# Kernel optimization log

Hardware: AMD Instinct MI355X
Metric: run time of the kernel (lower is better)

## Reference

```python
import jax, jax.numpy as jnp
import numpy as np

B, T, N, D, K, MP = 32, 50, 50000, 128, 16, 50
HID = (D + K) // 2  # WP_1 out features


def _normalize(x, axis=-1, eps=1e-12):
    return x / jnp.maximum(jnp.linalg.norm(x, axis=axis, keepdims=True), eps)


def _layer_norm(x, g, b, eps=1e-6):
    m = jnp.mean(x, axis=-1, keepdims=True)
    v = jnp.var(x, axis=-1, keepdims=True)
    return (x - m) * jax.lax.rsqrt(v + eps) * g + b


def setup_inputs() -> dict:
    key = jax.random.key(0)
    ks = jax.random.split(key, 20)
    std = 0.01
    session = jax.random.randint(ks[0], (B, T), 1, N + 1)  # ids >= 1, no padding
    lengths = jnp.full((B,), T, dtype=jnp.int32)
    isValidSession = jnp.ones((B * T,), dtype=bool)
    inp = {
        'session': session,
        'lengths': lengths,
        'tau': 1,
        'isValidSession': isValidSession,
        'train': 1,
        'I_emb': jax.random.normal(ks[1], (N + 1, D)) * std,
        'P_emb': jax.random.normal(ks[2], (K, D)) * std,
        'E_P_emb': jax.random.normal(ks[3], (MP, D)) * std,
        'E_S_emb': jax.random.normal(ks[4], (MP + 1, D)) * std,
        'V': _normalize(jax.random.normal(ks[5], (K, D))),
        'WP1': jax.random.normal(ks[6], (HID, D)),   # torch Linear weight [out, in]
        'WP2': jax.random.normal(ks[7], (K, HID)),
        'Wq': jax.random.normal(ks[8], (D, D)) / np.sqrt(D),
        'Wk': jax.random.normal(ks[9], (D, D)) / np.sqrt(D),
        'Wv': jax.random.normal(ks[10], (D, D)) / np.sqrt(D),
        'Wo': jax.random.normal(ks[11], (D, D)) / np.sqrt(D),
        'FF1': jax.random.normal(ks[12], (D, D)) / np.sqrt(D),
        'FF2': jax.random.normal(ks[13], (D, D)) / np.sqrt(D),
        'ln1_g': jnp.ones((D,)), 'ln1_b': jnp.zeros((D,)),
        'ln2_g': jnp.ones((D,)), 'ln2_b': jnp.zeros((D,)),
    }
    return inp


def _forward(session, lengths, tau, I_emb, P_emb, E_P_emb, E_S_emb, V,
             WP1, WP2, Wq, Wk, Wv, Wo, FF1, FF2, ln1_g, ln1_b, ln2_g, ln2_b):
    Vn = _normalize(V)                               # forward renormalizes V rows
    lf = lengths.astype(jnp.float32)
    isValidPos = (session != 0).astype(jnp.float32)  # [B,T]
    sess_emb = I_emb[session]                        # [B,T,D]
    EP = E_P_emb[jnp.arange(T) + (MP - T)]           # [T,D]
    es_idx = jnp.maximum(jnp.arange(T)[None, :] + 1 - (T - lengths[:, None]), 0)
    ES = E_S_emb[es_idx]                             # [B,T,D]

    # ---- ProxySelection (dropout in eval mode = identity) ----
    X = isValidPos[..., None] * (sess_emb + EP[None])
    X = jax.nn.leaky_relu(X @ WP1.T, 0.1) @ WP2.T    # [B,T,K]
    fP = jnp.sum(X, axis=1) / lf[:, None]
    pi = jax.nn.softmax(fP / tau, axis=-1)           # [B,K]
    p_s = pi @ P_emb                                 # [B,D]
    v = _normalize(pi @ Vn)                          # [B,D]

    # ---- SIE: single-layer self-attention encoder ----
    Xs = sess_emb + ES
    subseq = jnp.triu(jnp.ones((T, T), dtype=bool), 1)[None]        # causal
    pad = (session == 0)[:, None, :]                                # key padding
    mask = (subseq | pad)
    mask = mask.at[:, :, 0].set(False)
    non_pad = (session != 0).astype(jnp.float32)[..., None]
    q, kk, vv = Xs @ Wq.T, Xs @ Wk.T, Xs @ Wv.T
    scores = jnp.einsum('btd,bsd->bts', q, kk) / np.sqrt(D)
    scores = jnp.where(mask, -1e9, scores)
    attn = jax.nn.softmax(scores, axis=-1)
    h = (attn @ vv) @ Wo.T
    h = _layer_norm(h + Xs, ln1_g, ln1_b) * non_pad
    f = jax.nn.relu(h @ FF1.T) @ FF2.T
    s_s = _layer_norm(f + h, ln2_g, ln2_b) * non_pad                # [B,T,D]

    # project out v component per sample
    s_s_proj = s_s - v[:, None, :] * jnp.sum(v[:, None, :] * s_s, axis=-1, keepdims=True)
    orthogonal = jnp.abs(jnp.sum(v * p_s, axis=-1)) / jnp.linalg.norm(p_s, axis=-1)

    # ---- train_phase: dist(p_s+s_s_proj[b,t], I_proj_b) for all items ----
    # I_proj_b = I - v_b (v_b . I); with ||v_b||=1:
    #   ||F - I_proj||^2 = ||F||^2 - 2(F.I - (F.v)(v.I)) + ||I||^2 - (v.I)^2
    F = p_s[:, None, :] + s_s_proj                   # [B,T,D]
    vI = jnp.einsum('nd,bd->bn', I_emb, v)           # [B,N+1]
    Fv = jnp.einsum('btd,bd->bt', F, v)              # [B,T]
    FI = jnp.einsum('btd,nd->btn', F, I_emb)         # [B,T,N+1]
    Fn2 = jnp.sum(F * F, axis=-1)                    # [B,T]
    In2 = jnp.sum(I_emb * I_emb, axis=-1)[None, :] - vI * vI  # [B,N+1]
    dist = Fn2[..., None] - 2.0 * (FI - Fv[..., None] * vI[:, None, :]) + In2[:, None, :]
    return dist.reshape(B * T, N + 1), orthogonal


def reference(session, lengths, tau, isValidSession, train,
              I_emb, P_emb, E_P_emb, E_S_emb, V,
              WP1, WP2, Wq, Wk, Wv, Wo, FF1, FF2, ln1_g, ln1_b, ln2_g, ln2_b):
    # isValidSession is all-True and train=1: distance rows = all (b,t) pairs
    return _forward(session, lengths, tau, I_emb, P_emb, E_P_emb, E_S_emb, V,
                    WP1, WP2, Wq, Wk, Wv, Wo, FF1, FF2, ln1_g, ln1_b, ln2_g, ln2_b)
```

## Files before the change

### kernel.cpp

```cpp
#include <hip/hip_runtime.h>
#include <math.h>

#define B   32
#define T   50
#define N1  50001
#define D   128
#define KP  16
#define MP  50
#define HID 72
#define BT  (B*T)

typedef __attribute__((ext_vector_type(8))) short short8v;
typedef __attribute__((ext_vector_type(4))) float f32x4;

__device__ __forceinline__ unsigned short f2bf(float x) {
    unsigned u = __float_as_uint(x);
    u += 0x7fffu + ((u >> 16) & 1u);
    return (unsigned short)(u >> 16);
}

__device__ __forceinline__ float blockReduceSum128(float val, volatile float* sbuf) {
    for (int off = 32; off > 0; off >>= 1) val += __shfl_down(val, off, 64);
    __syncthreads();
    if ((threadIdx.x & 63) == 0) sbuf[threadIdx.x >> 6] = val;
    __syncthreads();
    return sbuf[0] + sbuf[1];
}

__global__ void k_fused_emb(const int* __restrict__ session,
                            const int* __restrict__ lengths,
                            const float* __restrict__ I_emb,
                            const float* __restrict__ EP_emb,
                            const float* __restrict__ ES_emb,
                            const float* __restrict__ WP1,
                            const float* __restrict__ WP2,
                            const float* __restrict__ Wq,
                            const float* __restrict__ Wk,
                            const float* __restrict__ Wv,
                            float* __restrict__ X2,
                            float* __restrict__ xs_o, float* __restrict__ q_o,
                            float* __restrict__ k_o, float* __restrict__ v_o) {
    int bt = blockIdx.x; int b = bt / T; int t = bt % T;
    int tid = threadIdx.x;
    __shared__ __align__(16) float x[D];
    __shared__ __align__(16) float xs[D];
    __shared__ float h[HID];
    int sid = session[bt];
    float ie = I_emb[(size_t)sid * D + tid];
    float xv_ = (sid != 0) ? (ie + EP_emb[(t + MP - T) * D + tid]) : 0.f;
    int es = t + 1 - (T - lengths[b]); if (es < 0) es = 0;
    float xsv = ie + ES_emb[es * D + tid];
    x[tid] = xv_;
    xs[tid] = xsv;
    __syncthreads();
    float aq = 0.f, ak = 0.f, av = 0.f;
    {
        const float4* wq4 = (const float4*)(Wq + tid * D);
        const float4* wk4 = (const float4*)(Wk + tid * D);
        const float4* wv4 = (const float4*)(Wv + tid * D);
        const float4* x4  = (const float4*)xs;
        #pragma unroll 8
        for (int k = 0; k < D / 4; ++k) {
            float4 xv = x4[k];
            float4 a = wq4[k], bq = wk4[k], c = wv4[k];
            aq += xv.x * a.x + xv.y * a.y + xv.z * a.z + xv.w * a.w;
            ak += xv.x * bq.x + xv.y * bq.y + xv.z * bq.z + xv.w * bq.w;
            av += xv.x * c.x + xv.y * c.y + xv.z * c.z + xv.w * c.w;
        }
    }
    if (tid < HID) {
        float acc = 0.f;
        const float4* w4 = (const float4*)(WP1 + tid * D);
        const float4* x4 = (const float4*)x;
        #pragma unroll 8
        for (int k = 0; k < D / 4; ++k) {
            float4 w = w4[k]; float4 xv = x4[k];
            acc += xv.x * w.x + xv.y * w.y + xv.z * w.z + xv.w * w.w;
        }
        h[tid] = acc > 0.f ? acc : 0.1f * acc;
    }
    xs_o[bt * D + tid] = xsv;
    q_o[bt * D + tid] = aq; k_o[bt * D + tid] = ak; v_o[bt * D + tid] = av;
    __syncthreads();
    if (tid < KP) {
        float acc = 0.f;
        const float* w = WP2 + tid * HID;
        for (int k = 0; k < HID; ++k) acc += h[k] * w[k];
        X2[bt * KP + tid] = acc;
    }
}

__global__ void k_proxy_head(const float* __restrict__ X2,
                             const int* __restrict__ lengths,
                             const int* __restrict__ tau_i,
                             const float* __restrict__ P_emb,
                             const float* __restrict__ V,
                             float* __restrict__ ps_o,
                             float* __restrict__ v_o,
                             float* __restrict__ orth_o) {
    int b = blockIdx.x; int tid = threadIdx.x;
    __shared__ float pi[KP];
    __shared__ float vn[KP];
    __shared__ float sbuf[2];
    float tau = (float)tau_i[0];
    float lf = (float)lengths[b];
    if (tid < KP) {
        float s = 0.f;
        for (int t = 0; t < T; ++t) s += X2[(b * T + t) * KP + tid];
        pi[tid] = (s / lf) / tau;
    }
    if (tid < KP) {
        float s = 0.f;
        for (int d = 0; d < D; ++d) { float z = V[tid * D + d]; s += z * z; }
        vn[tid] = fmaxf(sqrtf(s), 1e-12f);
    }
    __syncthreads();
    if (tid == 0) {
        float m = pi[0];
        for (int k = 1; k < KP; ++k) m = fmaxf(m, pi[k]);
        float s = 0.f;
        for (int k = 0; k < KP; ++k) { float e = expf(pi[k] - m); pi[k] = e; s += e; }
        for (int k = 0; k < KP; ++k) pi[k] /= s;
    }
    __syncthreads();
    float p = 0.f, vt = 0.f;
    for (int k = 0; k < KP; ++k) {
        p  += pi[k] * P_emb[k * D + tid];
        vt += pi[k] * (V[k * D + tid] / vn[k]);
    }
    float vsq = blockReduceSum128(vt * vt, sbuf);
    float vv = vt / fmaxf(sqrtf(vsq), 1e-12f);
    float psq = blockReduceSum128(p * p, sbuf);
    float dvp = blockReduceSum128(vv * p, sbuf);
    ps_o[b * D + tid] = p;
    v_o[b * D + tid] = vv;
    if (tid == 0) orth_o[b] = fabsf(dvp) / sqrtf(psq);
}

__global__ void k_fused_attn(const int* __restrict__ session,
                             const float* __restrict__ q,
                             const float* __restrict__ kk,
                             const float* __restrict__ vv,
                             const float* __restrict__ xs,
                             const float* __restrict__ Wo,
                             const float* __restrict__ g1, const float* __restrict__ b1,
                             const float* __restrict__ FF1, const float* __restrict__ FF2,
                             const float* __restrict__ g2, const float* __restrict__ b2,
                             const float* __restrict__ ps, const float* __restrict__ v,
                             short* __restrict__ G16, float* __restrict__ Fn2) {
    int bt = blockIdx.x; int b = bt / T; int t = bt % T;
    int tid = threadIdx.x;
    __shared__ __align__(16) float qs[D];
    __shared__ __align__(16) float buf1[D];
    __shared__ __align__(16) float buf2[D];
    __shared__ float attn[64];
    __shared__ float sbuf[2];
    qs[tid] = q[bt * D + tid];
    __syncthreads();
    if (tid < T) {
        int s = tid;
        bool allowed = (s == 0) || ((s <= t) && (session[b * T + s] != 0));
        float sc = -1e9f;
        if (allowed) {
            float a = 0.f;
            const float4* kr = (const float4*)(kk + (size_t)(b * T + s) * D);
            const float4* q4 = (const float4*)qs;
            #pragma unroll 8
            for (int d = 0; d < D / 4; ++d) {
                float4 kv = kr[d]; float4 qv = q4[d];
                a += qv.x * kv.x + qv.y * kv.y + qv.z * kv.z + qv.w * kv.w;
            }
            sc = a * 0.088388347648318447f;
        }
        attn[s] = sc;
    }
    __syncthreads();
    if (tid < 64) {
        float vsc = (tid < T) ? attn[tid] : -1e30f;
        float m = vsc;
        for (int off = 32; off > 0; off >>= 1) m = fmaxf(m, __shfl_xor(m, off, 64));
        float e = (tid < T) ? expf(vsc - m) : 0.f;
        float ssum = e;
        for (int off = 32; off > 0; off >>= 1) ssum += __shfl_xor(ssum, off, 64);
        if (tid < T) attn[tid] = e / ssum;
    }
    __syncthreads();
    float acc = 0.f;
    for (int s = 0; s < T; ++s) acc += attn[s] * vv[(size_t)(b * T + s) * D + tid];
    buf1[tid] = acc;
    __syncthreads();
    float a = 0.f;
    {
        const float4* w4 = (const float4*)(Wo + tid * D);
        const float4* h4 = (const float4*)buf1;
        #pragma unroll 8
        for (int k = 0; k < D / 4; ++k) {
            float4 w = w4[k]; float4 hv = h4[k];
            a += hv.x * w.x + hv.y * w.y + hv.z * w.z + hv.w * w.w;
        }
    }
    float x1 = a + xs[bt * D + tid];
    float mean = blockReduceSum128(x1, sbuf) * (1.f / D);
    float dx = x1 - mean;
    float var = blockReduceSum128(dx * dx, sbuf) * (1.f / D);
    float hx = (dx * rsqrtf(var + 1e-6f) * g1[tid] + b1[tid]) * ((session[bt] != 0) ? 1.f : 0.f);
    buf2[tid] = hx;
    __syncthreads();
    float a1 = 0.f;
    {
        const float4* w4 = (const float4*)(FF1 + tid * D);
        const float4* h4 = (const float4*)buf2;
        #pragma unroll 8
        for (int k = 0; k < D / 4; ++k) {
            float4 w = w4[k]; float4 hv = h4[k];
            a1 += hv.x * w.x + hv.y * w.y + hv.z * w.z + hv.w * w.w;
        }
    }
    __syncthreads();
    buf1[tid] = fmaxf(a1, 0.f);
    __syncthreads();
    float f = 0.f;
    {
        const float4* w4 = (const float4*)(FF2 + tid * D);
        const float4* t4 = (const float4*)buf1;
        #pragma unroll 8
        for (int k = 0; k < D / 4; ++k) {
            float4 w = w4[k]; float4 tv = t4[k];
            f += tv.x * w.x + tv.y * w.y + tv.z * w.z + tv.w * w.w;
        }
    }
    float x2 = f + hx;
    float mean2 = blockReduceSum128(x2, sbuf) * (1.f / D);
    float dx2 = x2 - mean2;
    float var2 = blockReduceSum128(dx2 * dx2, sbuf) * (1.f / D);
    float ss = dx2 * rsqrtf(var2 + 1e-6f) * g2[tid] + b2[tid];
    ss *= (session[bt] != 0) ? 1.f : 0.f;
    float vb = v[b * D + tid];
    float vs = blockReduceSum128(vb * ss, sbuf);
    float ssp = ss - vb * vs;
    float Fd = ps[b * D + tid] + ssp;
    float Fv = blockReduceSum128(Fd * vb, sbuf);
    float Gd = Fd - Fv * vb;
    float fn2 = blockReduceSum128(Fd * Fd, sbuf);
    G16[bt * D + tid] = (short)f2bf(Gd);
    if (tid == 0) Fn2[bt] = fn2;
}

#define LDK 136

__global__ __launch_bounds__(256) void k_item_mfma(const float* __restrict__ I,
                                                   const float* __restrict__ v,
                                                   float* __restrict__ In2pb,
                                                   unsigned short* __restrict__ I16) {
    __shared__ __align__(16) short Is[64][LDK];
    __shared__ __align__(16) short Vs[32][LDK];
    __shared__ float sq[64][4];
    __shared__ float in2[64];
    int n0 = blockIdx.x * 64;
    int tid = threadIdx.x;
    {
        int vr = tid >> 3;
        int vc = (tid & 7) * 16;
        const float4* src = (const float4*)&v[vr * D + vc];
        #pragma unroll
        for (int s = 0; s < 4; ++s) {
            float4 f = src[s];
            ushort4 u;
            u.x = f2bf(f.x); u.y = f2bf(f.y); u.z = f2bf(f.z); u.w = f2bf(f.w);
            *(ushort4*)&Vs[vr][vc + s * 4] = u;
        }
    }
    {
        int r = tid >> 2;
        int qq = tid & 3;
        int n = n0 + r;
        float ss = 0.f;
        if (n < N1) {
            const float4* src = (const float4*)&I[(size_t)n * D + qq * 32];
            #pragma unroll
            for (int s = 0; s < 8; ++s) {
                float4 f = src[s];
                ss += f.x * f.x + f.y * f.y + f.z * f.z + f.w * f.w;
                ushort4 u;
                u.x = f2bf(f.x); u.y = f2bf(f.y); u.z = f2bf(f.z); u.w = f2bf(f.w);
                *(ushort4*)&Is[r][qq * 32 + s * 4] = u;
                *(ushort4*)&I16[(size_t)n * D + qq * 32 + s * 4] = u;
            }
        } else {
            #pragma unroll
            for (int s = 0; s < 8; ++s)
                *(ushort4*)&Is[r][qq * 32 + s * 4] = make_ushort4(0, 0, 0, 0);
        }
        sq[r][qq] = ss;
    }
    __syncthreads();
    if (tid < 64) in2[tid] = sq[tid][0] + sq[tid][1] + sq[tid][2] + sq[tid][3];
    __syncthreads();
    int w = tid >> 6, l = tid & 63, lr = l & 15, lg = l >> 4;
    f32x4 acc[2] = {{0.f,0.f,0.f,0.f},{0.f,0.f,0.f,0.f}};
    short8v af[4];
    #pragma unroll
    for (int ks = 0; ks < 4; ++ks)
        af[ks] = *(const short8v*)&Is[w * 16 + lr][ks * 32 + lg * 8];
    #pragma unroll
    for (int nt = 0; nt < 2; ++nt) {
        #pragma unroll
        for (int ks = 0; ks < 4; ++ks) {
            short8v bf = *(const short8v*)&Vs[nt * 16 + lr][ks * 32 + lg * 8];
            acc[nt] = __builtin_amdgcn_mfma_f32_16x16x32_bf16(af[ks], bf, acc[nt], 0, 0, 0);
        }
    }
    #pragma unroll
    for (int nt = 0; nt < 2; ++nt) {
        int b = nt * 16 + lr;
        #pragma unroll
        for (int i = 0; i < 4; ++i) {
            int item = w * 16 + lg * 4 + i;
            int n = n0 + item;
            if (n < N1) {
                float dvi = acc[nt][i];
                In2pb[(size_t)b * N1 + n] = in2[item] - dvi * dvi;
            }
        }
    }
}

#define BN 128
__global__ __launch_bounds__(256) void k_dist_mfma(const short* __restrict__ G16,
                                                   const unsigned short* __restrict__ I16,
                                                   const float* __restrict__ Fn2,
                                                   const float* __restrict__ In2pb,
                                                   float* __restrict__ out) {
    __shared__ __align__(16) short Bs[BN][LDK];
    __shared__ float in2s[B][BN];
    int n0  = blockIdx.x * BN;
    int rt0 = (blockIdx.y == 0) ? 0 : 7;
    int rt1 = (blockIdx.y == 0) ? 7 : 13;
    int tid = threadIdx.x;
    {
        int r  = tid >> 1;
        int c0 = (tid & 1) * 64;
        int n = n0 + r;
        #pragma unroll
        for (int s = 0; s < 8; ++s) {
            short8v bv = {};
            if (n < N1) bv = *(const short8v*)&I16[(size_t)n * D + c0 + s * 8];
            *(short8v*)&Bs[r][c0 + s * 8] = bv;
        }
    }
    for (int i = tid; i < B * BN; i += 256) {
        int bb = i >> 7;
        int cl = i & (BN - 1);
        int col = n0 + cl;
        in2s[bb][cl] = (col < N1) ? In2pb[(size_t)bb * N1 + col] : 0.f;
    }
    __syncthreads();
    int w  = tid >> 6;
    int l  = tid & 63;
    int lr = l & 15;
    int lg = l >> 4;
    for (int rt = rt0; rt < rt1; ++rt) {
        int bt0 = rt * 128;
        #pragma unroll
        for (int mi = 0; mi < 2; ++mi) {
            int rbase = bt0 + w * 32 + mi * 16;
            short8v af[4];
            const short* arow = &G16[(size_t)(rbase + lr) * D];
            #pragma unroll
            for (int ks = 0; ks < 4; ++ks)
                af[ks] = *(const short8v*)&arow[ks * 32 + lg * 8];
            f32x4 acc[8];
            #pragma unroll
            for (int nt = 0; nt < 8; ++nt) acc[nt] = (f32x4){0.f, 0.f, 0.f, 0.f};
            #pragma unroll
            for (int nt = 0; nt < 8; ++nt) {
                #pragma unroll
                for (int ks = 0; ks < 4; ++ks) {
                    short8v bf = *(const short8v*)&Bs[nt * 16 + lr][ks * 32 + lg * 8];
                    acc[nt] = __builtin_amdgcn_mfma_f32_16x16x32_bf16(af[ks], bf, acc[nt], 0, 0, 0);
                }
            }
            int rb = rbase + lg * 4;
            if (rb < BT) {
                float4 fn4 = *(const float4*)&Fn2[rb];
                float fnv[4] = {fn4.x, fn4.y, fn4.z, fn4.w};
                #pragma unroll
                for (int i = 0; i < 4; ++i) {
                    int row = rb + i;
                    int bb = row / T;
                    float* orow = out + (size_t)row * N1 + n0;
                    #pragma unroll
                    for (int nt = 0; nt < 8; ++nt) {
                        int cl = nt * 16 + lr;
                        if (n0 + cl < N1) orow[cl] = fnv[i] + in2s[bb][cl] - 2.f * acc[nt][i];
                    }
                }
            }
        }
    }
}

extern "C" void kernel_launch(void* const* d_in, const int* in_sizes, int n_in,
                              void* d_out, int out_size, void* d_ws, size_t ws_size,
                              hipStream_t stream) {
    const int*   session = (const int*)d_in[0];
    const int*   lengths = (const int*)d_in[1];
    const int*   tau     = (const int*)d_in[2];
    const float* I_emb   = (const float*)d_in[5];
    const float* P_emb   = (const float*)d_in[6];
    const float* EP      = (const float*)d_in[7];
    const float* ES      = (const float*)d_in[8];
    const float* V       = (const float*)d_in[9];
    const float* WP1     = (const float*)d_in[10];
    const float* WP2     = (const float*)d_in[11];
    const float* Wq      = (const float*)d_in[12];
    const float* Wk      = (const float*)d_in[13];
    const float* Wv      = (const float*)d_in[14];
    const float* Wo      = (const float*)d_in[15];
    const float* FF1     = (const float*)d_in[16];
    const float* FF2     = (const float*)d_in[17];
    const float* g1      = (const float*)d_in[18];
    const float* b1      = (const float*)d_in[19];
    const float* g2      = (const float*)d_in[20];
    const float* b2      = (const float*)d_in[21];
    float* out = (float*)d_out;
    float* ws  = (float*)d_ws;

    float* wsX2   = ws;
    float* wsPs   = wsX2 + 25600;
    float* wsV    = wsPs + 4096;
    float* wsXs   = wsV + 4096;
    float* wsQ    = wsXs + 204800;
    float* wsK    = wsQ + 204800;
    float* wsVv   = wsK + 204800;
    float* wsFn2  = wsVv + 204800;
    float* wsIn2  = wsFn2 + 1600;
    short* wsG16  = (short*)(wsIn2 + 1600032);
    unsigned short* wsI16 = (unsigned short*)(wsG16 + 212992);

    float* orth_out = out + (size_t)BT * N1;

    k_fused_emb <<<BT, 128, 0, stream>>>(session, lengths, I_emb, EP, ES,
                                         WP1, WP2, Wq, Wk, Wv,
                                         wsX2, wsXs, wsQ, wsK, wsVv);
    k_proxy_head<<<B, 128, 0, stream>>>(wsX2, lengths, tau, P_emb, V, wsPs, wsV, orth_out);
    k_fused_attn<<<BT, 128, 0, stream>>>(session, wsQ, wsK, wsVv, wsXs,
                                         Wo, g1, b1, FF1, FF2, g2, b2,
                                         wsPs, wsV, wsG16, wsFn2);
    k_item_mfma <<<(N1 + 63) / 64, 256, 0, stream>>>(I_emb, wsV, wsIn2, wsI16);
    dim3 gdist((N1 + BN - 1) / BN, 2);
    k_dist_mfma <<<gdist, 256, 0, stream>>>(wsG16, wsI16, wsFn2, wsIn2, out);
}
```

Baseline: 265.2 us.

## Fuse embedding, proxy head and transformer layer into one per-batch kernel

Replaces three kernels (per-position embedding/QKV, per-batch proxy head, per-position attention+FFN) with one kernel launched once per batch element, 256 threads each. All intermediates (xs, q, k, v, hidden, attention output) stay in LDS. Each weight row is reused across 10 sequence positions per tile. This removes two launches and the global round-trips for Q/K/V/X2/ps. The cost is that parallelism drops to 32 blocks, several stages use only 16–128 of the 256 threads, and the kernel needs a large LDS footprint, so this part may run serially on a few CUs.

```diff
diff --git a/kernel.cpp b/kernel.cpp
--- a/kernel.cpp
+++ b/kernel.cpp
@@ -19,231 +19,303 @@
     return (unsigned short)(u >> 16);
 }
 
-__device__ __forceinline__ float blockReduceSum128(float val, volatile float* sbuf) {
-    for (int off = 32; off > 0; off >>= 1) val += __shfl_down(val, off, 64);
-    __syncthreads();
-    if ((threadIdx.x & 63) == 0) sbuf[threadIdx.x >> 6] = val;
-    __syncthreads();
-    return sbuf[0] + sbuf[1];
+__device__ __forceinline__ float halfReduce256(float v, int half, int lane, volatile float* rbuf) {
+    for (int off = 32; off > 0; off >>= 1) v += __shfl_down(v, off, 64);
+    __syncthreads();
+    if ((lane & 63) == 0) rbuf[half * 2 + (lane >> 6)] = v;
+    __syncthreads();
+    return rbuf[half * 2] + rbuf[half * 2 + 1];
 }
 
-__global__ void k_fused_emb(const int* __restrict__ session,
-                            const int* __restrict__ lengths,
-                            const float* __restrict__ I_emb,
-                            const float* __restrict__ EP_emb,
-                            const float* __restrict__ ES_emb,
-                            const float* __restrict__ WP1,
-                            const float* __restrict__ WP2,
-                            const float* __restrict__ Wq,
-                            const float* __restrict__ Wk,
-                            const float* __restrict__ Wv,
-                            float* __restrict__ X2,
-                            float* __restrict__ xs_o, float* __restrict__ q_o,
-                            float* __restrict__ k_o, float* __restrict__ v_o) {
-    int bt = blockIdx.x; int b = bt / T; int t = bt % T;
+__global__ __launch_bounds__(256) void k_mega(const int* __restrict__ session,
+                                              const int* __restrict__ lengths,
+                                              const int* __restrict__ tau_i,
+                                              const float* __restrict__ I_emb,
+                                              const float* __restrict__ EP,
+                                              const float* __restrict__ ES,
+                                              const float* __restrict__ WP1,
+                                              const float* __restrict__ WP2,
+                                              const float* __restrict__ P_emb,
+                                              const float* __restrict__ V,
+                                              const float* __restrict__ Wq,
+                                              const float* __restrict__ Wk,
+                                              const float* __restrict__ Wv,
+                                              const float* __restrict__ Wo,
+                                              const float* __restrict__ g1, const float* __restrict__ b1,
+                                              const float* __restrict__ FF1, const float* __restrict__ FF2,
+                                              const float* __restrict__ g2, const float* __restrict__ b2,
+                                              short* __restrict__ G16,
+                                              float* __restrict__ Fn2,
+                                              float* __restrict__ v_o,
+                                              float* __restrict__ orth_o) {
+    __shared__ __align__(16) float xsS[T][132];
+    __shared__ __align__(16) float qS[T][132];
+    __shared__ __align__(16) float kS[T][132];
+    __shared__ __align__(16) float vS[T][132];
+    __shared__ __align__(16) float aoS[T][132];
+    __shared__ __align__(16) float hS[T][76];
+    __shared__ float X2S[T][KP];
+    __shared__ float attnS[2][64];
+    __shared__ float psS[D];
+    __shared__ float vvS[D];
+    __shared__ float piS[KP];
+    __shared__ float vnS[KP];
+    __shared__ int   sessS[T];
+    __shared__ float rbuf[4];
+
+    int b = blockIdx.x;
     int tid = threadIdx.x;
-    __shared__ __align__(16) float x[D];
-    __shared__ __align__(16) float xs[D];
-    __shared__ float h[HID];
-    int sid = session[bt];
-    float ie = I_emb[(size_t)sid * D + tid];
-    float xv_ = (sid != 0) ? (ie + EP_emb[(t + MP - T) * D + tid]) : 0.f;
-    int es = t + 1 - (T - lengths[b]); if (es < 0) es = 0;
-    float xsv = ie + ES_emb[es * D + tid];
-    x[tid] = xv_;
-    xs[tid] = xsv;
-    __syncthreads();
-    float aq = 0.f, ak = 0.f, av = 0.f;
-    {
-        const float4* wq4 = (const float4*)(Wq + tid * D);
-        const float4* wk4 = (const float4*)(Wk + tid * D);
-        const float4* wv4 = (const float4*)(Wv + tid * D);
-        const float4* x4  = (const float4*)xs;
-        #pragma unroll 8
-        for (int k = 0; k < D / 4; ++k) {
-            float4 xv = x4[k];
-            float4 a = wq4[k], bq = wk4[k], c = wv4[k];
-            aq += xv.x * a.x + xv.y * a.y + xv.z * a.z + xv.w * a.w;
-            ak += xv.x * bq.x + xv.y * bq.y + xv.z * bq.z + xv.w * bq.w;
-            av += xv.x * c.x + xv.y * c.y + xv.z * c.z + xv.w * c.w;
-        }
-    }
-    if (tid < HID) {
-        float acc = 0.f;
-        const float4* w4 = (const float4*)(WP1 + tid * D);
-        const float4* x4 = (const float4*)x;
-        #pragma unroll 8
-        for (int k = 0; k < D / 4; ++k) {
-            float4 w = w4[k]; float4 xv = x4[k];
-            acc += xv.x * w.x + xv.y * w.y + xv.z * w.z + xv.w * w.w;
-        }
-        h[tid] = acc > 0.f ? acc : 0.1f * acc;
-    }
-    xs_o[bt * D + tid] = xsv;
-    q_o[bt * D + tid] = aq; k_o[bt * D + tid] = ak; v_o[bt * D + tid] = av;
-    __syncthreads();
-    if (tid < KP) {
-        float acc = 0.f;
-        const float* w = WP2 + tid * HID;
-        for (int k = 0; k < HID; ++k) acc += h[k] * w[k];
-        X2[bt * KP + tid] = acc;
-    }
-}
-
-__global__ void k_proxy_head(const float* __restrict__ X2,
-                             const int* __restrict__ lengths,
-                             const int* __restrict__ tau_i,
-                             const float* __restrict__ P_emb,
-                             const float* __restrict__ V,
-                             float* __restrict__ ps_o,
-                             float* __restrict__ v_o,
-                             float* __restrict__ orth_o) {
-    int b = blockIdx.x; int tid = threadIdx.x;
-    __shared__ float pi[KP];
-    __shared__ float vn[KP];
-    __shared__ float sbuf[2];
+    int half = tid >> 7;
+    int lane = tid & 127;
+    if (tid < T) sessS[tid] = session[b * T + tid];
+    int len = lengths[b];
+    __syncthreads();
+
+    for (int t = 0; t < T; t += 2) {
+        int pos = t + half;
+        int sid = sessS[pos];
+        float ie = I_emb[(size_t)sid * D + lane];
+        float xv = (sid != 0) ? (ie + EP[(pos + MP - T) * D + lane]) : 0.f;
+        int es = pos + 1 - (T - len); if (es < 0) es = 0;
+        xsS[pos][lane] = ie + ES[es * D + lane];
+        aoS[pos][lane] = xv;
+    }
+    __syncthreads();
+
+    for (int r = tid; r < HID; r += 256) {
+        const float4* wrow = (const float4*)(WP1 + r * D);
+        for (int tile = 0; tile < 5; ++tile) {
+            float acc[10];
+            #pragma unroll
+            for (int j = 0; j < 10; ++j) acc[j] = 0.f;
+            for (int c = 0; c < 32; ++c) {
+                float4 w = wrow[c];
+                #pragma unroll
+                for (int j = 0; j < 10; ++j) {
+                    float4 xv = *(const float4*)&aoS[tile * 10 + j][c * 4];
+                    acc[j] += xv.x * w.x + xv.y * w.y + xv.z * w.z + xv.w * w.w;
+                }
+            }
+            #pragma unroll
+            for (int j = 0; j < 10; ++j) {
+                float a = acc[j];
+                hS[tile * 10 + j][r] = a > 0.f ? a : 0.1f * a;
+            }
+        }
+    }
+    __syncthreads();
+
+    for (int r = tid; r < KP; r += 256) {
+        const float4* wrow = (const float4*)(WP2 + r * HID);
+        for (int tile = 0; tile < 5; ++tile) {
+            float acc[10];
+            #pragma unroll
+            for (int j = 0; j < 10; ++j) acc[j] = 0.f;
+            for (int c = 0; c < 18; ++c) {
+                float4 w = wrow[c];
+                #pragma unroll
+                for (int j = 0; j < 10; ++j) {
+                    float4 xv = *(const float4*)&hS[tile * 10 + j][c * 4];
+                    acc[j] += xv.x * w.x + xv.y * w.y + xv.z * w.z + xv.w * w.w;
+                }
+            }
+            #pragma unroll
+            for (int j = 0; j < 10; ++j) X2S[tile * 10 + j][r] = acc[j];
+        }
+    }
+    __syncthreads();
+
     float tau = (float)tau_i[0];
-    float lf = (float)lengths[b];
+    float lf = (float)len;
     if (tid < KP) {
         float s = 0.f;
-        for (int t = 0; t < T; ++t) s += X2[(b * T + t) * KP + tid];
-        pi[tid] = (s / lf) / tau;
-    }
-    if (tid < KP) {
+        for (int t = 0; t < T; ++t) s += X2S[t][tid];
+        piS[tid] = (s / lf) / tau;
+        float sn = 0.f;
+        for (int d = 0; d < D; ++d) { float z = V[tid * D + d]; sn += z * z; }
+        vnS[tid] = fmaxf(sqrtf(sn), 1e-12f);
+    }
+    __syncthreads();
+    if (tid == 0) {
+        float m = piS[0];
+        for (int k = 1; k < KP; ++k) m = fmaxf(m, piS[k]);
         float s = 0.f;
-        for (int d = 0; d < D; ++d) { float z = V[tid * D + d]; s += z * z; }
-        vn[tid] = fmaxf(sqrtf(s), 1e-12f);
-    }
-    __syncthreads();
-    if (tid == 0) {
-        float m = pi[0];
-        for (int k = 1; k < KP; ++k) m = fmaxf(m, pi[k]);
-        float s = 0.f;
-        for (int k = 0; k < KP; ++k) { float e = expf(pi[k] - m); pi[k] = e; s += e; }
-        for (int k = 0; k < KP; ++k) pi[k] /= s;
-    }
-    __syncthreads();
-    float p = 0.f, vt = 0.f;
-    for (int k = 0; k < KP; ++k) {
-        p  += pi[k] * P_emb[k * D + tid];
-        vt += pi[k] * (V[k * D + tid] / vn[k]);
-    }
-    float vsq = blockReduceSum128(vt * vt, sbuf);
-    float vv = vt / fmaxf(sqrtf(vsq), 1e-12f);
-    float psq = blockReduceSum128(p * p, sbuf);
-    float dvp = blockReduceSum128(vv * p, sbuf);
-    ps_o[b * D + tid] = p;
-    v_o[b * D + tid] = vv;
-    if (tid == 0) orth_o[b] = fabsf(dvp) / sqrtf(psq);
-}
-
-__global__ void k_fused_attn(const int* __restrict__ session,
-                             const float* __restrict__ q,
-                             const float* __restrict__ kk,
-                             const float* __restrict__ vv,
-                             const float* __restrict__ xs,
-                             const float* __restrict__ Wo,
-                             const float* __restrict__ g1, const float* __restrict__ b1,
-                             const float* __restrict__ FF1, const float* __restrict__ FF2,
-                             const float* __restrict__ g2, const float* __restrict__ b2,
-                             const float* __restrict__ ps, const float* __restrict__ v,
-                             short* __restrict__ G16, float* __restrict__ Fn2) {
-    int bt = blockIdx.x; int b = bt / T; int t = bt % T;
-    int tid = threadIdx.x;
-    __shared__ __align__(16) float qs[D];
-    __shared__ __align__(16) float buf1[D];
-    __shared__ __align__(16) float buf2[D];
-    __shared__ float attn[64];
-    __shared__ float sbuf[2];
-    qs[tid] = q[bt * D + tid];
-    __syncthreads();
-    if (tid < T) {
-        int s = tid;
-        bool allowed = (s == 0) || ((s <= t) && (session[b * T + s] != 0));
-        float sc = -1e9f;
-        if (allowed) {
-            float a = 0.f;
-            const float4* kr = (const float4*)(kk + (size_t)(b * T + s) * D);
-            const float4* q4 = (const float4*)qs;
-            #pragma unroll 8
-            for (int d = 0; d < D / 4; ++d) {
-                float4 kv = kr[d]; float4 qv = q4[d];
-                a += qv.x * kv.x + qv.y * kv.y + qv.z * kv.z + qv.w * kv.w;
-            }
-            sc = a * 0.088388347648318447f;
-        }
-        attn[s] = sc;
-    }
-    __syncthreads();
-    if (tid < 64) {
-        float vsc = (tid < T) ? attn[tid] : -1e30f;
-        float m = vsc;
-        for (int off = 32; off > 0; off >>= 1) m = fmaxf(m, __shfl_xor(m, off, 64));
-        float e = (tid < T) ? expf(vsc - m) : 0.f;
-        float ssum = e;
-        for (int off = 32; off > 0; off >>= 1) ssum += __shfl_xor(ssum, off, 64);
-        if (tid < T) attn[tid] = e / ssum;
-    }
-    __syncthreads();
-    float acc = 0.f;
-    for (int s = 0; s < T; ++s) acc += attn[s] * vv[(size_t)(b * T + s) * D + tid];
-    buf1[tid] = acc;
-    __syncthreads();
-    float a = 0.f;
+        for (int k = 0; k < KP; ++k) { float e = expf(piS[k] - m); piS[k] = e; s += e; }
+        for (int k = 0; k < KP; ++k) piS[k] /= s;
+    }
+    __syncthreads();
     {
-        const float4* w4 = (const float4*)(Wo + tid * D);
-        const float4* h4 = (const float4*)buf1;
-        #pragma unroll 8
-        for (int k = 0; k < D / 4; ++k) {
-            float4 w = w4[k]; float4 hv = h4[k];
-            a += hv.x * w.x + hv.y * w.y + hv.z * w.z + hv.w * w.w;
-        }
-    }
-    float x1 = a + xs[bt * D + tid];
-    float mean = blockReduceSum128(x1, sbuf) * (1.f / D);
-    float dx = x1 - mean;
-    float var = blockReduceSum128(dx * dx, sbuf) * (1.f / D);
-    float hx = (dx * rsqrtf(var + 1e-6f) * g1[tid] + b1[tid]) * ((session[bt] != 0) ? 1.f : 0.f);
-    buf2[tid] = hx;
-    __syncthreads();
-    float a1 = 0.f;
-    {
-        const float4* w4 = (const float4*)(FF1 + tid * D);
-        const float4* h4 = (const float4*)buf2;
-        #pragma unroll 8
-        for (int k = 0; k < D / 4; ++k) {
-            float4 w = w4[k]; float4 hv = h4[k];
-            a1 += hv.x * w.x + hv.y * w.y + hv.z * w.z + hv.w * w.w;
-        }
-    }
-    __syncthreads();
-    buf1[tid] = fmaxf(a1, 0.f);
-    __syncthreads();
-    float f = 0.f;
-    {
-        const float4* w4 = (const float4*)(FF2 + tid * D);
-        const float4* t4 = (const float4*)buf1;
-        #pragma unroll 8
-        for (int k = 0; k < D / 4; ++k) {
-            float4 w = w4[k]; float4 tv = t4[k];
-            f += tv.x * w.x + tv.y * w.y + tv.z * w.z + tv.w * w.w;
-        }
-    }
-    float x2 = f + hx;
-    float mean2 = blockReduceSum128(x2, sbuf) * (1.f / D);
-    float dx2 = x2 - mean2;
-    float var2 = blockReduceSum128(dx2 * dx2, sbuf) * (1.f / D);
-    float ss = dx2 * rsqrtf(var2 + 1e-6f) * g2[tid] + b2[tid];
-    ss *= (session[bt] != 0) ? 1.f : 0.f;
-    float vb = v[b * D + tid];
-    float vs = blockReduceSum128(vb * ss, sbuf);
-    float ssp = ss - vb * vs;
-    float Fd = ps[b * D + tid] + ssp;
-    float Fv = blockReduceSum128(Fd * vb, sbuf);
-    float Gd = Fd - Fv * vb;
-    float fn2 = blockReduceSum128(Fd * Fd, sbuf);
-    G16[bt * D + tid] = (short)f2bf(Gd);
-    if (tid == 0) Fn2[bt] = fn2;
+        float p = 0.f, vt = 0.f;
+        if (tid < D) {
+            for (int k = 0; k < KP; ++k) {
+                p  += piS[k] * P_emb[k * D + tid];
+                vt += piS[k] * (V[k * D + tid] / vnS[k]);
+            }
+        }
+        float vsq = halfReduce256(vt * vt, half, lane, rbuf);
+        float vv = (tid < D) ? vt / fmaxf(sqrtf(vsq), 1e-12f) : 0.f;
+        float psq = halfReduce256(p * p, half, lane, rbuf);
+        float dvp = halfReduce256(vv * p, half, lane, rbuf);
+        if (tid < D) {
+            psS[tid] = p;
+            vvS[tid] = vv;
+            v_o[b * D + tid] = vv;
+        }
+        if (tid == 0) orth_o[b] = fabsf(dvp) / sqrtf(psq);
+    }
+    __syncthreads();
+
+    for (int r = tid; r < 384; r += 256) {
+        int m = r >> 7, row = r & 127;
+        const float* W = (m == 0) ? Wq : ((m == 1) ? Wk : Wv);
+        const float4* wrow = (const float4*)(W + row * D);
+        float (*dst)[132] = (m == 0) ? qS : ((m == 1) ? kS : vS);
+        for (int tile = 0; tile < 5; ++tile) {
+            float acc[10];
+            #pragma unroll
+            for (int j = 0; j < 10; ++j) acc[j] = 0.f;
+            for (int c = 0; c < 32; ++c) {
+                float4 w = wrow[c];
+                #pragma unroll
+                for (int j = 0; j < 10; ++j) {
+                    float4 xv = *(const float4*)&xsS[tile * 10 + j][c * 4];
+                    acc[j] += xv.x * w.x + xv.y * w.y + xv.z * w.z + xv.w * w.w;
+                }
+            }
+            #pragma unroll
+            for (int j = 0; j < 10; ++j) dst[tile * 10 + j][row] = acc[j];
+        }
+    }
+    __syncthreads();
+
+    for (int t = 0; t < T; t += 2) {
+        int pos = t + half;
+        if (lane < T) {
+            int s = lane;
+            bool allowed = (s == 0) || ((s <= pos) && (sessS[s] != 0));
+            float sc = -1e9f;
+            if (allowed) {
+                float a = 0.f;
+                const float4* kr = (const float4*)kS[s];
+                const float4* q4 = (const float4*)qS[pos];
+                #pragma unroll 8
+                for (int d = 0; d < 32; ++d) {
+                    float4 kv = kr[d]; float4 qv = q4[d];
+                    a += qv.x * kv.x + qv.y * kv.y + qv.z * kv.z + qv.w * kv.w;
+                }
+                sc = a * 0.088388347648318447f;
+            }
+            attnS[half][s] = sc;
+        }
+        __syncthreads();
+        if (lane < 64) {
+            float vsc = (lane < T) ? attnS[half][lane] : -1e30f;
+            float m = vsc;
+            for (int off = 32; off > 0; off >>= 1) m = fmaxf(m, __shfl_xor(m, off, 64));
+            float e = (lane < T) ? expf(vsc - m) : 0.f;
+            float ssum = e;
+            for (int off = 32; off > 0; off >>= 1) ssum += __shfl_xor(ssum, off, 64);
+            if (lane < T) attnS[half][lane] = e / ssum;
+        }
+        __syncthreads();
+        float ao = 0.f;
+        for (int s = 0; s < T; ++s) ao += attnS[half][s] * vS[s][lane];
+        __syncthreads();
+        aoS[pos][lane] = ao;
+    }
+    __syncthreads();
+
+    for (int r = tid; r < D; r += 256) {
+        const float4* wrow = (const float4*)(Wo + r * D);
+        for (int tile = 0; tile < 5; ++tile) {
+            float acc[10];
+            #pragma unroll
+            for (int j = 0; j < 10; ++j) acc[j] = 0.f;
+            for (int c = 0; c < 32; ++c) {
+                float4 w = wrow[c];
+                #pragma unroll
+                for (int j = 0; j < 10; ++j) {
+                    float4 xv = *(const float4*)&aoS[tile * 10 + j][c * 4];
+                    acc[j] += xv.x * w.x + xv.y * w.y + xv.z * w.z + xv.w * w.w;
+                }
+            }
+            #pragma unroll
+            for (int j = 0; j < 10; ++j) kS[tile * 10 + j][r] = acc[j];
+        }
+    }
+    __syncthreads();
+
+    for (int t = 0; t < T; t += 2) {
+        int pos = t + half;
+        float x1 = kS[pos][lane] + xsS[pos][lane];
+        float mean = halfReduce256(x1, half, lane, rbuf) * (1.f / D);
+        float dx = x1 - mean;
+        float var = halfReduce256(dx * dx, half, lane, rbuf) * (1.f / D);
+        float nonpad = (sessS[pos] != 0) ? 1.f : 0.f;
+        float hx = (dx * rsqrtf(var + 1e-6f) * g1[lane] + b1[lane]) * nonpad;
+        aoS[pos][lane] = hx;
+    }
+    __syncthreads();
+
+    for (int r = tid; r < D; r += 256) {
+        const float4* wrow = (const float4*)(FF1 + r * D);
+        for (int tile = 0; tile < 5; ++tile) {
+            float acc[10];
+            #pragma unroll
+            for (int j = 0; j < 10; ++j) acc[j] = 0.f;
+            for (int c = 0; c < 32; ++c) {
+                float4 w = wrow[c];
+                #pragma unroll
+                for (int j = 0; j < 10; ++j) {
+                    float4 xv = *(const float4*)&aoS[tile * 10 + j][c * 4];
+                    acc[j] += xv.x * w.x + xv.y * w.y + xv.z * w.z + xv.w * w.w;
+                }
+            }
+            #pragma unroll
+            for (int j = 0; j < 10; ++j) qS[tile * 10 + j][r] = fmaxf(acc[j], 0.f);
+        }
+    }
+    __syncthreads();
+
+    for (int r = tid; r < D; r += 256) {
+        const float4* wrow = (const float4*)(FF2 + r * D);
+        for (int tile = 0; tile < 5; ++tile) {
+            float acc[10];
+            #pragma unroll
+            for (int j = 0; j < 10; ++j) acc[j] = 0.f;
+            for (int c = 0; c < 32; ++c) {
+                float4 w = wrow[c];
+                #pragma unroll
+                for (int j = 0; j < 10; ++j) {
+                    float4 xv = *(const float4*)&qS[tile * 10 + j][c * 4];
+                    acc[j] += xv.x * w.x + xv.y * w.y + xv.z * w.z + xv.w * w.w;
+                }
+            }
+            #pragma unroll
+            for (int j = 0; j < 10; ++j) kS[tile * 10 + j][r] = acc[j];
+        }
+    }
+    __syncthreads();
+
+    for (int t = 0; t < T; t += 2) {
+        int pos = t + half;
+        float hx = aoS[pos][lane];
+        float x2 = kS[pos][lane] + hx;
+        float mean = halfReduce256(x2, half, lane, rbuf) * (1.f / D);
+        float dx = x2 - mean;
+        float var = halfReduce256(dx * dx, half, lane, rbuf) * (1.f / D);
+        float nonpad = (sessS[pos] != 0) ? 1.f : 0.f;
+        float ss = (dx * rsqrtf(var + 1e-6f) * g2[lane] + b2[lane]) * nonpad;
+        float vb = vvS[lane];
+        float vs = halfReduce256(vb * ss, half, lane, rbuf);
+        float ssp = ss - vb * vs;
+        float Fd = psS[lane] + ssp;
+        float Fv = halfReduce256(Fd * vb, half, lane, rbuf);
+        float fn2 = halfReduce256(Fd * Fd, half, lane, rbuf);
+        float Gd = Fd - Fv * vb;
+        G16[(size_t)(b * T + pos) * D + lane] = (short)f2bf(Gd);
+        if (lane == 0) Fn2[b * T + pos] = fn2;
+    }
 }
 
 #define LDK 136
@@ -426,28 +498,19 @@
     float* out = (float*)d_out;
     float* ws  = (float*)d_ws;
 
-    float* wsX2   = ws;
-    float* wsPs   = wsX2 + 25600;
-    float* wsV    = wsPs + 4096;
-    float* wsXs   = wsV + 4096;
-    float* wsQ    = wsXs + 204800;
-    float* wsK    = wsQ + 204800;
-    float* wsVv   = wsK + 204800;
-    float* wsFn2  = wsVv + 204800;
+    float* wsV    = ws;
+    float* wsFn2  = wsV + 4096;
     float* wsIn2  = wsFn2 + 1600;
     short* wsG16  = (short*)(wsIn2 + 1600032);
     unsigned short* wsI16 = (unsigned short*)(wsG16 + 212992);
 
     float* orth_out = out + (size_t)BT * N1;
 
-    k_fused_emb <<<BT, 128, 0, stream>>>(session, lengths, I_emb, EP, ES,
-                                         WP1, WP2, Wq, Wk, Wv,
-                                         wsX2, wsXs, wsQ, wsK, wsVv);
-    k_proxy_head<<<B, 128, 0, stream>>>(wsX2, lengths, tau, P_emb, V, wsPs, wsV, orth_out);
-    k_fused_attn<<<BT, 128, 0, stream>>>(session, wsQ, wsK, wsVv, wsXs,
-                                         Wo, g1, b1, FF1, FF2, g2, b2,
-                                         wsPs, wsV, wsG16, wsFn2);
-    k_item_mfma <<<(N1 + 63) / 64, 256, 0, stream>>>(I_emb, wsV, wsIn2, wsI16);
+    k_mega<<<B, 256, 0, stream>>>(session, lengths, tau, I_emb, EP, ES,
+                                  WP1, WP2, P_emb, V, Wq, Wk, Wv, Wo,
+                                  g1, b1, FF1, FF2, g2, b2,
+                                  wsG16, wsFn2, wsV, orth_out);
+    k_item_mfma<<<(N1 + 63) / 64, 256, 0, stream>>>(I_emb, wsV, wsIn2, wsI16);
     dim3 gdist((N1 + BN - 1) / BN, 2);
-    k_dist_mfma <<<gdist, 256, 0, stream>>>(wsG16, wsI16, wsFn2, wsIn2, out);
+    k_dist_mfma<<<gdist, 256, 0, stream>>>(wsG16, wsI16, wsFn2, wsIn2, out);
 }
```

Result: slower. 493.6 us (+86.1%).
